# Kernel tuning notes

Hardware: AMD Instinct MI355X
Metric: run time of the kernel (lower is better)

Reference implementation:

```python
import jax, jax.numpy as jnp
import numpy as np

N, T, D, H = 64, 512, 1024, 1024

def setup_inputs() -> dict:
    key = jax.random.key(0)
    k1, k2, k3, k4 = jax.random.split(key, 4)
    x = jax.random.normal(k1, (N, T, D), dtype=jnp.float32)
    h0 = jax.random.normal(k2, (N, H), dtype=jnp.float32)
    Wx = jax.random.normal(k3, (D, H), dtype=jnp.float32) / np.sqrt(D)
    Wh = jax.random.normal(k4, (H, H), dtype=jnp.float32) / np.sqrt(H)
    b = jnp.zeros((H,), dtype=jnp.float32)
    return {"x": x, "h0": h0, "Wx": Wx, "Wh": Wh, "b": b}

def reference(x, h0, Wx, Wh, b):
    # Precompute input projection for all timesteps in one big GEMM: (N,T,D)@(D,H) -> (N,T,H)
    xW = jnp.einsum('ntd,dh->nth', x, Wx) + b
    xW_t = jnp.swapaxes(xW, 0, 1)  # (T, N, H)

    def step(prev_h, xw):
        next_h = jnp.tanh(prev_h @ Wh + xw)
        return next_h, next_h

    _, h_t = jax.lax.scan(step, h0, xW_t)  # h_t: (T, N, H)
    return jnp.swapaxes(h_t, 0, 1)  # (N, T, H)
```

## Files before the change

kernel.cpp:

```cpp
#include <hip/hip_runtime.h>

#define NB 64
#define TT 512
#define DD 1024
#define HH 1024

typedef unsigned long long u64;
typedef __attribute__((ext_vector_type(4))) float f32x4;
typedef __attribute__((ext_vector_type(8))) short bf16x8;

static __device__ __forceinline__ unsigned short f2bf(float f) {
  unsigned u = __float_as_uint(f);
  unsigned r = (u + 0x7fffu + ((u >> 16) & 1u)) >> 16;
  return (unsigned short)r;
}
static __device__ __forceinline__ float bf2f(unsigned short u) {
  return __uint_as_float(((unsigned)u) << 16);
}
static __device__ __forceinline__ float ftanh(float x) {
  float z = __builtin_amdgcn_exp2f(x * 2.8853900817779268f);
  return 1.f - 2.f * __builtin_amdgcn_rcpf(z + 1.f);
}
static __device__ __forceinline__ void async_copy16(void* lds, const void* g) {
  __builtin_amdgcn_global_load_lds(
      (const __attribute__((address_space(1))) unsigned int*)g,
      (__attribute__((address_space(3))) unsigned int*)lds, 16, 0, 0);
}

__global__ __launch_bounds__(256) void prep_kernel(
    const float* __restrict__ x, const float* __restrict__ Wx,
    const float* __restrict__ h0, unsigned short* __restrict__ Wxh,
    unsigned short* __restrict__ Wxl, unsigned short* __restrict__ hbuf0,
    unsigned short* __restrict__ xbf, int nx, int permuted) {
  __shared__ float tile[32][33];
  int b = blockIdx.x;
  int tid = threadIdx.x;
  if (b < nx) {
    int g = b * 256 + tid;
    int r = g >> 7, jb = g & 127;
    int q = jb >> 3, j = jb & 7;
    const float4* src = (const float4*)(x + r * 1024 + jb * 8);
    float4 a0 = src[0], a1 = src[1];
    uint4 o;
    o.x = (unsigned)f2bf(a0.x) | ((unsigned)f2bf(a0.y) << 16);
    o.y = (unsigned)f2bf(a0.z) | ((unsigned)f2bf(a0.w) << 16);
    o.z = (unsigned)f2bf(a1.x) | ((unsigned)f2bf(a1.y) << 16);
    o.w = (unsigned)f2bf(a1.z) | ((unsigned)f2bf(a1.w) << 16);
    *(uint4*)((char*)xbf + (size_t)r * 2048 + q * 128 + ((j ^ (r & 7)) << 4)) = o;
  } else if (b < nx + 1024) {
    int bb = b - nx;
    int tk = (bb & 31) * 32;
    int tn = (bb >> 5) * 32;
    int tx = tid & 31;
    int ty = tid >> 5;
#pragma unroll
    for (int ii = 0; ii < 4; ++ii) {
      int kk = ty + ii * 8;
      tile[kk][tx] = Wx[(tk + kk) * HH + tn + tx];
    }
    __syncthreads();
#pragma unroll
    for (int ii = 0; ii < 4; ++ii) {
      int a = ty + ii * 8;
      float wv = tile[tx][a];
      unsigned short hi = f2bf(wv);
      float lo = wv - bf2f(hi);
      int c = tn + a, k = tk + tx;
      int idx;
      if (permuted) {
        int qq = k >> 6, e = k & 63, j = e >> 3;
        idx = c * 1024 + qq * 64 + ((j ^ (c & 7)) << 3) + (e & 7);
      } else {
        idx = c * 1024 + k;
      }
      Wxh[idx] = hi;
      Wxl[idx] = f2bf(lo);
    }
  } else {
    int i = (b - nx - 1024) * 256 + tid;
    int n = i >> 7, cb = i & 127;
    const float4* s4 = (const float4*)(h0 + n * 1024 + cb * 8);
    float4 a0 = s4[0], a1 = s4[1];
    uint4 o;
    o.x = (unsigned)f2bf(a0.x) | ((unsigned)f2bf(a0.y) << 16);
    o.y = (unsigned)f2bf(a0.z) | ((unsigned)f2bf(a0.w) << 16);
    o.z = (unsigned)f2bf(a1.x) | ((unsigned)f2bf(a1.y) << 16);
    o.w = (unsigned)f2bf(a1.z) | ((unsigned)f2bf(a1.w) << 16);
    *(uint4*)((char*)hbuf0 + (size_t)n * 2048 + cb * 16) = o;
  }
}

__global__ __launch_bounds__(256) void xw_gemm_fast(
    const unsigned short* __restrict__ xbf,
    const unsigned short* __restrict__ Wxh,
    const unsigned short* __restrict__ Wxl, const float* __restrict__ bias,
    float* __restrict__ out) {
  __shared__ unsigned short As[128 * 64];
  __shared__ unsigned short Bh[128 * 64];
  __shared__ unsigned short Bl[128 * 64];
  int tid = threadIdx.x;
  int w = tid >> 6, lane = tid & 63;
  int n0 = blockIdx.x * 128, row0 = blockIdx.y * 128;
  int wr = w >> 1, wc = w & 1;

  f32x4 acc[4][4];
#pragma unroll
  for (int m = 0; m < 4; ++m)
#pragma unroll
    for (int n = 0; n < 4; ++n) acc[m][n] = (f32x4)0.f;

  const char* xb = (const char*)xbf;
  const char* hb = (const char*)Wxh;
  const char* lb = (const char*)Wxl;

  for (int kc = 0; kc < 16; ++kc) {
    __syncthreads();
#pragma unroll
    for (int i = 0; i < 4; ++i) {
      int ub = i * 4096 + w * 1024;
      int off = ub + lane * 16;
      int r = off >> 7, inrow = off & 127;
      async_copy16((char*)As + ub,
                   xb + (size_t)(row0 + r) * 2048 + kc * 128 + inrow);
    }
#pragma unroll
    for (int i = 0; i < 4; ++i) {
      int ub = i * 4096 + w * 1024;
      int off = ub + lane * 16;
      int c = off >> 7, inrow = off & 127;
      async_copy16((char*)Bh + ub,
                   hb + (size_t)(n0 + c) * 2048 + kc * 128 + inrow);
      async_copy16((char*)Bl + ub,
                   lb + (size_t)(n0 + c) * 2048 + kc * 128 + inrow);
    }
    asm volatile("s_waitcnt vmcnt(0)" ::: "memory");
    __syncthreads();
#pragma unroll
    for (int kt = 0; kt < 2; ++kt) {
      int krel2 = (kt * 32 + ((lane >> 4) << 3)) * 2;
      bf16x8 af[4], bhf[4], blf[4];
#pragma unroll
      for (int m = 0; m < 4; ++m) {
        int r = wr * 64 + m * 16 + (lane & 15);
        af[m] = *(const bf16x8*)((const char*)As + r * 128 +
                                 (krel2 ^ ((r & 7) << 4)));
      }
#pragma unroll
      for (int n = 0; n < 4; ++n) {
        int c = wc * 64 + n * 16 + (lane & 15);
        int off = c * 128 + (krel2 ^ ((c & 7) << 4));
        bhf[n] = *(const bf16x8*)((const char*)Bh + off);
        blf[n] = *(const bf16x8*)((const char*)Bl + off);
      }
#pragma unroll
      for (int m = 0; m < 4; ++m)
#pragma unroll
        for (int n = 0; n < 4; ++n) {
          acc[m][n] = __builtin_amdgcn_mfma_f32_16x16x32_bf16(af[m], bhf[n],
                                                              acc[m][n], 0, 0, 0);
          acc[m][n] = __builtin_amdgcn_mfma_f32_16x16x32_bf16(af[m], blf[n],
                                                              acc[m][n], 0, 0, 0);
        }
    }
  }

#pragma unroll
  for (int n = 0; n < 4; ++n) {
    int col = n0 + wc * 64 + n * 16 + (lane & 15);
    float bv = bias[col];
#pragma unroll
    for (int m = 0; m < 4; ++m) {
      int rbase = row0 + wr * 64 + m * 16 + ((lane >> 4) << 2);
#pragma unroll
      for (int i = 0; i < 4; ++i)
        out[(size_t)(rbase + i) * HH + col] = acc[m][n][i] + bv;
    }
  }
}

__global__ __launch_bounds__(256) void xw_gemm_slow(
    const float* __restrict__ x, const unsigned short* __restrict__ Wxh,
    const unsigned short* __restrict__ Wxl, const float* __restrict__ bias,
    float* __restrict__ out) {
  __shared__ unsigned short As[128 * 64];
  __shared__ unsigned short Bh[128 * 64];
  __shared__ unsigned short Bl[128 * 64];

  int tid = threadIdx.x;
  int n0 = blockIdx.x * 128;
  int row0 = blockIdx.y * 128;
  int w = tid >> 6, lane = tid & 63;
  int wr = w >> 1, wc = w & 1;

  f32x4 acc[4][4];
#pragma unroll
  for (int m = 0; m < 4; ++m)
#pragma unroll
    for (int n = 0; n < 4; ++n) acc[m][n] = (f32x4)0.f;

  for (int kk = 0; kk < DD; kk += 64) {
    float4 av[8];
#pragma unroll
    for (int i = 0; i < 8; ++i) {
      int lin = tid + 256 * i;
      int r = lin >> 4, kq = lin & 15;
      av[i] = *(const float4*)(x + (size_t)(row0 + r) * DD + kk + kq * 4);
    }
    int4 bhv[4], blv[4];
#pragma unroll
    for (int i = 0; i < 4; ++i) {
      int lin = tid + 256 * i;
      int c = lin >> 3, kb = lin & 7;
      bhv[i] = *(const int4*)(Wxh + (size_t)(n0 + c) * DD + kk + kb * 8);
      blv[i] = *(const int4*)(Wxl + (size_t)(n0 + c) * DD + kk + kb * 8);
    }
    __syncthreads();
#pragma unroll
    for (int i = 0; i < 8; ++i) {
      int lin = tid + 256 * i;
      int r = lin >> 4, kq = lin & 15;
      uint2 u;
      u.x = (unsigned)f2bf(av[i].x) | ((unsigned)f2bf(av[i].y) << 16);
      u.y = (unsigned)f2bf(av[i].z) | ((unsigned)f2bf(av[i].w) << 16);
      *(uint2*)((char*)As + r * 128 + ((kq * 8) ^ ((r & 7) << 4))) = u;
    }
#pragma unroll
    for (int i = 0; i < 4; ++i) {
      int lin = tid + 256 * i;
      int c = lin >> 3, kb = lin & 7;
      int off = c * 128 + ((kb * 16) ^ ((c & 7) << 4));
      *(int4*)((char*)Bh + off) = bhv[i];
      *(int4*)((char*)Bl + off) = blv[i];
    }
    __syncthreads();
#pragma unroll
    for (int kt = 0; kt < 2; ++kt) {
      int krel2 = (kt * 32 + ((lane >> 4) << 3)) * 2;
      bf16x8 af[4], bhf[4], blf[4];
#pragma unroll
      for (int m = 0; m < 4; ++m) {
        int r = wr * 64 + m * 16 + (lane & 15);
        af[m] = *(const bf16x8*)((const char*)As + r * 128 +
                                 (krel2 ^ ((r & 7) << 4)));
      }
#pragma unroll
      for (int n = 0; n < 4; ++n) {
        int c = wc * 64 + n * 16 + (lane & 15);
        int off = c * 128 + (krel2 ^ ((c & 7) << 4));
        bhf[n] = *(const bf16x8*)((const char*)Bh + off);
        blf[n] = *(const bf16x8*)((const char*)Bl + off);
      }
#pragma unroll
      for (int m = 0; m < 4; ++m)
#pragma unroll
        for (int n = 0; n < 4; ++n) {
          acc[m][n] = __builtin_amdgcn_mfma_f32_16x16x32_bf16(af[m], bhf[n],
                                                              acc[m][n], 0, 0, 0);
          acc[m][n] = __builtin_amdgcn_mfma_f32_16x16x32_bf16(af[m], blf[n],
                                                              acc[m][n], 0, 0, 0);
        }
    }
    __syncthreads();
  }

#pragma unroll
  for (int n = 0; n < 4; ++n) {
    int col = n0 + wc * 64 + n * 16 + (lane & 15);
    float bv = bias[col];
#pragma unroll
    for (int m = 0; m < 4; ++m) {
      int rbase = row0 + wr * 64 + m * 16 + ((lane >> 4) << 2);
#pragma unroll
      for (int i = 0; i < 4; ++i)
        out[(size_t)(rbase + i) * HH + col] = acc[m][n][i] + bv;
    }
  }
}

__global__ __launch_bounds__(256) void rnn_scan(
    const float* __restrict__ Wh, float* __restrict__ out,
    unsigned short* __restrict__ hbuf, unsigned* __restrict__ flags) {
  int tid = threadIdx.x;
  int w = tid >> 6, lane = tid & 63;
  int p = blockIdx.x >> 4;
  int q = blockIdx.x & 15;
  int n0 = p * 16;
  int c0 = q * 64;

  __shared__ float red[2][4][16][68];

  bf16x8 whi[4][8], wlo[4][8];
#pragma unroll
  for (int ct = 0; ct < 4; ++ct) {
#pragma unroll
    for (int kt = 0; kt < 8; ++kt) {
      int c = c0 + ct * 16 + (lane & 15);
      int kb = w * 256 + kt * 32 + ((lane >> 4) << 3);
#pragma unroll
      for (int j = 0; j < 8; ++j) {
        float wf = Wh[(size_t)(kb + j) * HH + c];
        unsigned short hi = f2bf(wf);
        whi[ct][kt][j] = (short)hi;
        wlo[ct][kt][j] = (short)f2bf(wf - bf2f(hi));
      }
    }
  }

  int erow_l = tid >> 4;
  int erow = n0 + erow_l;
  int ecol = c0 + ((tid & 15) << 2);
  size_t obase = (size_t)erow * (TT * HH) + ecol;
  int hbase = erow * HH + ecol;
  int abase = (n0 + (lane & 15)) * HH + w * 256 + ((lane >> 4) << 3);

  unsigned* myflag = flags + p * 64 + q * 4 + w;
  const unsigned* pollp = flags + p * 64 + lane;

  float4 xw0 = *(const float4*)(out + obase);
  float4 xw1 = *(const float4*)(out + obase + HH);
  float4 prev_hv = make_float4(0.f, 0.f, 0.f, 0.f);

  for (int t = 0; t < TT; ++t) {
    const unsigned short* hp = hbuf + (t & 1) * (NB * HH);
    unsigned short* hn = hbuf + ((t + 1) & 1) * (NB * HH);

    if (t > 0) {
      unsigned tg = (unsigned)t;
      for (;;) {
        unsigned v = __hip_atomic_load(pollp, __ATOMIC_RELAXED,
                                       __HIP_MEMORY_SCOPE_AGENT);
        if (__all((int)(v >= tg))) break;
        __builtin_amdgcn_s_sleep(1);
      }
      asm volatile("" ::: "memory");
    }

    const u64* hq = (const u64*)(hp + abase);
    u64 pu[8][2];
#pragma unroll
    for (int kt = 0; kt < 8; ++kt) {
      pu[kt][0] = __hip_atomic_load(hq + kt * 8, __ATOMIC_RELAXED,
                                    __HIP_MEMORY_SCOPE_AGENT);
      pu[kt][1] = __hip_atomic_load(hq + kt * 8 + 1, __ATOMIC_RELAXED,
                                    __HIP_MEMORY_SCOPE_AGENT);
    }

    f32x4 acc[4];
#pragma unroll
    for (int ct = 0; ct < 4; ++ct) acc[ct] = (f32x4)0.f;
#pragma unroll
    for (int kt = 0; kt < 8; ++kt) {
      union { u64 u[2]; bf16x8 v; } pk;
      pk.u[0] = pu[kt][0];
      pk.u[1] = pu[kt][1];
#pragma unroll
      for (int ct = 0; ct < 4; ++ct) {
        acc[ct] = __builtin_amdgcn_mfma_f32_16x16x32_bf16(pk.v, whi[ct][kt],
                                                          acc[ct], 0, 0, 0);
        acc[ct] = __builtin_amdgcn_mfma_f32_16x16x32_bf16(pk.v, wlo[ct][kt],
                                                          acc[ct], 0, 0, 0);
      }
    }

    int db = t & 1;
    int rr = (lane >> 4) << 2, cc = lane & 15;
#pragma unroll
    for (int ct = 0; ct < 4; ++ct)
#pragma unroll
      for (int i = 0; i < 4; ++i) red[db][w][rr + i][ct * 16 + cc] = acc[ct][i];
    asm volatile("s_waitcnt lgkmcnt(0)" ::: "memory");
    __builtin_amdgcn_s_barrier();
    asm volatile("" ::: "memory");

    int c4 = (tid & 15) << 2;
    float4 s = make_float4(0.f, 0.f, 0.f, 0.f);
#pragma unroll
    for (int ww = 0; ww < 4; ++ww) {
      float4 v = *(const float4*)&red[db][ww][erow_l][c4];
      s.x += v.x; s.y += v.y; s.z += v.z; s.w += v.w;
    }
    float4 hv;
    hv.x = ftanh(s.x + xw0.x);
    hv.y = ftanh(s.y + xw0.y);
    hv.z = ftanh(s.z + xw0.z);
    hv.w = ftanh(s.w + xw0.w);

    if (t + 1 < TT) {
      unsigned lo32 = (unsigned)f2bf(hv.x) | ((unsigned)f2bf(hv.y) << 16);
      unsigned hi32 = (unsigned)f2bf(hv.z) | ((unsigned)f2bf(hv.w) << 16);
      __hip_atomic_store((u64*)(hn + hbase), ((u64)hi32 << 32) | lo32,
                         __ATOMIC_RELAXED, __HIP_MEMORY_SCOPE_AGENT);
      asm volatile("s_waitcnt vmcnt(0)" ::: "memory");
      if (lane == 0)
        __hip_atomic_store(myflag, (unsigned)(t + 1), __ATOMIC_RELAXED,
                           __HIP_MEMORY_SCOPE_AGENT);
    }

    if (t > 0) *(float4*)(out + obase + (size_t)(t - 1) * HH) = prev_hv;
    prev_hv = hv;
    float4 xwf = make_float4(0.f, 0.f, 0.f, 0.f);
    if (t + 2 < TT) xwf = *(const float4*)(out + obase + (size_t)(t + 2) * HH);
    xw0 = xw1;
    xw1 = xwf;
  }
  *(float4*)(out + obase + (size_t)(TT - 1) * HH) = prev_hv;
}

extern "C" void kernel_launch(void* const* d_in, const int* in_sizes, int n_in,
                              void* d_out, int out_size, void* d_ws,
                              size_t ws_size, hipStream_t stream) {
  const float* x = (const float*)d_in[0];
  const float* h0 = (const float*)d_in[1];
  const float* Wx = (const float*)d_in[2];
  const float* Wh = (const float*)d_in[3];
  const float* b = (const float*)d_in[4];
  float* out = (float*)d_out;

  char* ws = (char*)d_ws;
  unsigned* flags = (unsigned*)ws;
  unsigned short* hbuf = (unsigned short*)(ws + 4096);
  unsigned short* Wxh = (unsigned short*)(ws + 266240);
  unsigned short* Wxl = (unsigned short*)(ws + 2363392);
  unsigned short* xbf = (unsigned short*)(ws + 4460544);

  int fast = (ws_size >= 71569408ULL) ? 1 : 0;
  int nx = fast ? 16384 : 0;

  hipMemsetAsync(flags, 0, 4096, stream);
  prep_kernel<<<nx + 1056, 256, 0, stream>>>(x, Wx, h0, Wxh, Wxl, hbuf, xbf,
                                             nx, fast);
  if (fast)
    xw_gemm_fast<<<dim3(8, 256), 256, 0, stream>>>(xbf, Wxh, Wxl, b, out);
  else
    xw_gemm_slow<<<dim3(8, 256), 256, 0, stream>>>(x, Wxh, Wxl, b, out);
  rnn_scan<<<64, 256, 0, stream>>>(Wh, out, hbuf, flags);
}
```

Measured before the change: 2.297 ms.

## Replace flag polling with timestamp-tagged hidden-state words in a 4-deep ring buffer

The separate per-wave flag array and its poll/store handshake are removed. Each 64-bit hidden-state word now carries two bf16 values in its low half and the timestep tag in its high half. Consumers spin on the data loads themselves until every tag matches, and the buffer becomes a 4-slot ring so a slot is not overwritten while slower blocks still read it. This drops a round trip and the vmcnt wait before each flag store on the serial critical path, at the cost of twice the hidden-state traffic and repeated re-reads of the full operand while spinning. The output store and the xw prefetch are also moved ahead of the MFMA work.

```diff
diff --git a/kernel.cpp b/kernel.cpp
--- a/kernel.cpp
+++ b/kernel.cpp
@@ -30,7 +30,7 @@
 __global__ __launch_bounds__(256) void prep_kernel(
     const float* __restrict__ x, const float* __restrict__ Wx,
     const float* __restrict__ h0, unsigned short* __restrict__ Wxh,
-    unsigned short* __restrict__ Wxl, unsigned short* __restrict__ hbuf0,
+    unsigned short* __restrict__ Wxl, u64* __restrict__ hbuf,
     unsigned short* __restrict__ xbf, int nx, int permuted) {
   __shared__ float tile[32][33];
   int b = blockIdx.x;
@@ -77,16 +77,13 @@
       Wxl[idx] = f2bf(lo);
     }
   } else {
-    int i = (b - nx - 1024) * 256 + tid;
-    int n = i >> 7, cb = i & 127;
-    const float4* s4 = (const float4*)(h0 + n * 1024 + cb * 8);
-    float4 a0 = s4[0], a1 = s4[1];
-    uint4 o;
-    o.x = (unsigned)f2bf(a0.x) | ((unsigned)f2bf(a0.y) << 16);
-    o.y = (unsigned)f2bf(a0.z) | ((unsigned)f2bf(a0.w) << 16);
-    o.z = (unsigned)f2bf(a1.x) | ((unsigned)f2bf(a1.y) << 16);
-    o.w = (unsigned)f2bf(a1.z) | ((unsigned)f2bf(a1.w) << 16);
-    *(uint4*)((char*)hbuf0 + (size_t)n * 2048 + cb * 16) = o;
+    int pi = (b - nx - 1024) * 256 + tid;
+    int n = pi >> 9, c2 = pi & 511;
+    float v0 = h0[n * HH + c2 * 2];
+    float v1 = h0[n * HH + c2 * 2 + 1];
+    unsigned lo32 = (unsigned)f2bf(v0) | ((unsigned)f2bf(v1) << 16);
+    __hip_atomic_store(hbuf + pi, (u64)lo32, __ATOMIC_RELAXED,
+                       __HIP_MEMORY_SCOPE_AGENT);
   }
 }
 
@@ -279,7 +276,7 @@
 
 __global__ __launch_bounds__(256) void rnn_scan(
     const float* __restrict__ Wh, float* __restrict__ out,
-    unsigned short* __restrict__ hbuf, unsigned* __restrict__ flags) {
+    u64* __restrict__ hbuf) {
   int tid = threadIdx.x;
   int w = tid >> 6, lane = tid & 63;
   int p = blockIdx.x >> 4;
@@ -310,54 +307,47 @@
   int erow = n0 + erow_l;
   int ecol = c0 + ((tid & 15) << 2);
   size_t obase = (size_t)erow * (TT * HH) + ecol;
-  int hbase = erow * HH + ecol;
-  int abase = (n0 + (lane & 15)) * HH + w * 256 + ((lane >> 4) << 3);
-
-  unsigned* myflag = flags + p * 64 + q * 4 + w;
-  const unsigned* pollp = flags + p * 64 + lane;
+  int pstore = (p * 16 + erow_l) * 512 + (ecol >> 1);
+  int pload = (p * 16 + (lane & 15)) * 512 + w * 128 + ((lane >> 4) << 2);
 
   float4 xw0 = *(const float4*)(out + obase);
   float4 xw1 = *(const float4*)(out + obase + HH);
   float4 prev_hv = make_float4(0.f, 0.f, 0.f, 0.f);
 
   for (int t = 0; t < TT; ++t) {
-    const unsigned short* hp = hbuf + (t & 1) * (NB * HH);
-    unsigned short* hn = hbuf + ((t + 1) & 1) * (NB * HH);
-
-    if (t > 0) {
-      unsigned tg = (unsigned)t;
-      for (;;) {
-        unsigned v = __hip_atomic_load(pollp, __ATOMIC_RELAXED,
-                                       __HIP_MEMORY_SCOPE_AGENT);
-        if (__all((int)(v >= tg))) break;
-        __builtin_amdgcn_s_sleep(1);
-      }
-      asm volatile("" ::: "memory");
-    }
-
-    const u64* hq = (const u64*)(hp + abase);
-    u64 pu[8][2];
+    const u64* hq = hbuf + (unsigned)(t & 3) * 32768 + pload;
+    u64* hn = hbuf + (unsigned)((t + 1) & 3) * 32768;
+    unsigned tg = (unsigned)t;
+
+    u64 pk[32];
+    for (;;) {
+#pragma unroll
+      for (int i = 0; i < 32; ++i)
+        pk[i] = __hip_atomic_load(hq + (i >> 2) * 16 + (i & 3),
+                                  __ATOMIC_RELAXED, __HIP_MEMORY_SCOPE_AGENT);
+      unsigned bad = 0;
+#pragma unroll
+      for (int i = 0; i < 32; ++i) bad |= (unsigned)(pk[i] >> 32) ^ tg;
+      if (__all((int)(bad == 0))) break;
+    }
+
+    if (t > 0) *(float4*)(out + obase + (size_t)(t - 1) * HH) = prev_hv;
+    float4 xwf = make_float4(0.f, 0.f, 0.f, 0.f);
+    if (t + 2 < TT) xwf = *(const float4*)(out + obase + (size_t)(t + 2) * HH);
+
+    f32x4 acc[4];
+#pragma unroll
+    for (int ct = 0; ct < 4; ++ct) acc[ct] = (f32x4)0.f;
 #pragma unroll
     for (int kt = 0; kt < 8; ++kt) {
-      pu[kt][0] = __hip_atomic_load(hq + kt * 8, __ATOMIC_RELAXED,
-                                    __HIP_MEMORY_SCOPE_AGENT);
-      pu[kt][1] = __hip_atomic_load(hq + kt * 8 + 1, __ATOMIC_RELAXED,
-                                    __HIP_MEMORY_SCOPE_AGENT);
-    }
-
-    f32x4 acc[4];
-#pragma unroll
-    for (int ct = 0; ct < 4; ++ct) acc[ct] = (f32x4)0.f;
-#pragma unroll
-    for (int kt = 0; kt < 8; ++kt) {
-      union { u64 u[2]; bf16x8 v; } pk;
-      pk.u[0] = pu[kt][0];
-      pk.u[1] = pu[kt][1];
+      union { unsigned u[4]; bf16x8 v; } pkk;
+#pragma unroll
+      for (int j = 0; j < 4; ++j) pkk.u[j] = (unsigned)pk[kt * 4 + j];
 #pragma unroll
       for (int ct = 0; ct < 4; ++ct) {
-        acc[ct] = __builtin_amdgcn_mfma_f32_16x16x32_bf16(pk.v, whi[ct][kt],
+        acc[ct] = __builtin_amdgcn_mfma_f32_16x16x32_bf16(pkk.v, whi[ct][kt],
                                                           acc[ct], 0, 0, 0);
-        acc[ct] = __builtin_amdgcn_mfma_f32_16x16x32_bf16(pk.v, wlo[ct][kt],
+        acc[ct] = __builtin_amdgcn_mfma_f32_16x16x32_bf16(pkk.v, wlo[ct][kt],
                                                           acc[ct], 0, 0, 0);
       }
     }
@@ -386,20 +376,15 @@
     hv.w = ftanh(s.w + xw0.w);
 
     if (t + 1 < TT) {
-      unsigned lo32 = (unsigned)f2bf(hv.x) | ((unsigned)f2bf(hv.y) << 16);
-      unsigned hi32 = (unsigned)f2bf(hv.z) | ((unsigned)f2bf(hv.w) << 16);
-      __hip_atomic_store((u64*)(hn + hbase), ((u64)hi32 << 32) | lo32,
-                         __ATOMIC_RELAXED, __HIP_MEMORY_SCOPE_AGENT);
-      asm volatile("s_waitcnt vmcnt(0)" ::: "memory");
-      if (lane == 0)
-        __hip_atomic_store(myflag, (unsigned)(t + 1), __ATOMIC_RELAXED,
-                           __HIP_MEMORY_SCOPE_AGENT);
-    }
-
-    if (t > 0) *(float4*)(out + obase + (size_t)(t - 1) * HH) = prev_hv;
+      u64 thi = ((u64)(unsigned)(t + 1)) << 32;
+      unsigned lo0 = (unsigned)f2bf(hv.x) | ((unsigned)f2bf(hv.y) << 16);
+      unsigned lo1 = (unsigned)f2bf(hv.z) | ((unsigned)f2bf(hv.w) << 16);
+      __hip_atomic_store(hn + pstore, thi | lo0, __ATOMIC_RELAXED,
+                         __HIP_MEMORY_SCOPE_AGENT);
+      __hip_atomic_store(hn + pstore + 1, thi | lo1, __ATOMIC_RELAXED,
+                         __HIP_MEMORY_SCOPE_AGENT);
+    }
     prev_hv = hv;
-    float4 xwf = make_float4(0.f, 0.f, 0.f, 0.f);
-    if (t + 2 < TT) xwf = *(const float4*)(out + obase + (size_t)(t + 2) * HH);
     xw0 = xw1;
     xw1 = xwf;
   }
@@ -417,21 +402,20 @@
   float* out = (float*)d_out;
 
   char* ws = (char*)d_ws;
-  unsigned* flags = (unsigned*)ws;
-  unsigned short* hbuf = (unsigned short*)(ws + 4096);
-  unsigned short* Wxh = (unsigned short*)(ws + 266240);
-  unsigned short* Wxl = (unsigned short*)(ws + 2363392);
-  unsigned short* xbf = (unsigned short*)(ws + 4460544);
-
-  int fast = (ws_size >= 71569408ULL) ? 1 : 0;
+  u64* hbuf = (u64*)(ws + 4096);
+  unsigned short* Wxh = (unsigned short*)(ws + 1052672);
+  unsigned short* Wxl = (unsigned short*)(ws + 3149824);
+  unsigned short* xbf = (unsigned short*)(ws + 5246976);
+
+  int fast = (ws_size >= 72355840ULL) ? 1 : 0;
   int nx = fast ? 16384 : 0;
 
-  hipMemsetAsync(flags, 0, 4096, stream);
-  prep_kernel<<<nx + 1056, 256, 0, stream>>>(x, Wx, h0, Wxh, Wxl, hbuf, xbf,
+  hipMemsetAsync(hbuf, 0, 1048576, stream);
+  prep_kernel<<<nx + 1152, 256, 0, stream>>>(x, Wx, h0, Wxh, Wxl, hbuf, xbf,
                                              nx, fast);
   if (fast)
     xw_gemm_fast<<<dim3(8, 256), 256, 0, stream>>>(xbf, Wxh, Wxl, b, out);
   else
     xw_gemm_slow<<<dim3(8, 256), 256, 0, stream>>>(x, Wxh, Wxl, b, out);
-  rnn_scan<<<64, 256, 0, stream>>>(Wh, out, hbuf, flags);
-}
+  rnn_scan<<<64, 256, 0, stream>>>(Wh, out, hbuf);
+}
```

Measured after the change: 3.198 ms. 39.2% more time.

## Aggregate per-block step flags via LDS counter and poll only dependent blocks

Applied to the files above, without the earlier changes.

Each block now publishes a single step flag. The last of its four waves to finish, found through an LDS atomic counter, writes it, instead of every wave writing its own flag. Each wave polls only the four producer blocks whose columns feed its K-slice, rather than all 64 wave flags of the batch group. This narrows the cross-block dependency and cuts polling traffic. The code also drops the two-step xW prefetch and the delayed output store, so the xW load and output store now happen inside each step. The output store is also now covered by the vmcnt(0) wait before the flag is published, which may lengthen the critical path.

```diff
diff --git a/kernel.cpp b/kernel.cpp
--- a/kernel.cpp
+++ b/kernel.cpp
@@ -288,6 +288,8 @@
   int c0 = q * 64;
 
   __shared__ float red[2][4][16][68];
+  __shared__ unsigned cnt;
+  if (tid == 0) cnt = 0u;
 
   bf16x8 whi[4][8], wlo[4][8];
 #pragma unroll
@@ -305,6 +307,7 @@
       }
     }
   }
+  __syncthreads();
 
   int erow_l = tid >> 4;
   int erow = n0 + erow_l;
@@ -313,12 +316,8 @@
   int hbase = erow * HH + ecol;
   int abase = (n0 + (lane & 15)) * HH + w * 256 + ((lane >> 4) << 3);
 
-  unsigned* myflag = flags + p * 64 + q * 4 + w;
-  const unsigned* pollp = flags + p * 64 + lane;
-
-  float4 xw0 = *(const float4*)(out + obase);
-  float4 xw1 = *(const float4*)(out + obase + HH);
-  float4 prev_hv = make_float4(0.f, 0.f, 0.f, 0.f);
+  unsigned* myflag = flags + p * 64 + q;
+  const unsigned* fp = flags + p * 64 + (w << 2);
 
   for (int t = 0; t < TT; ++t) {
     const unsigned short* hp = hbuf + (t & 1) * (NB * HH);
@@ -327,13 +326,17 @@
     if (t > 0) {
       unsigned tg = (unsigned)t;
       for (;;) {
-        unsigned v = __hip_atomic_load(pollp, __ATOMIC_RELAXED,
-                                       __HIP_MEMORY_SCOPE_AGENT);
-        if (__all((int)(v >= tg))) break;
+        unsigned fv = 0xFFFFFFFFu;
+        if (lane < 4)
+          fv = __hip_atomic_load(fp + lane, __ATOMIC_RELAXED,
+                                 __HIP_MEMORY_SCOPE_AGENT);
+        if (__all((int)(fv >= tg))) break;
         __builtin_amdgcn_s_sleep(1);
       }
       asm volatile("" ::: "memory");
     }
+
+    float4 xwc = *(const float4*)(out + obase + (size_t)t * HH);
 
     const u64* hq = (const u64*)(hp + abase);
     u64 pu[8][2];
@@ -380,10 +383,12 @@
       s.x += v.x; s.y += v.y; s.z += v.z; s.w += v.w;
     }
     float4 hv;
-    hv.x = ftanh(s.x + xw0.x);
-    hv.y = ftanh(s.y + xw0.y);
-    hv.z = ftanh(s.z + xw0.z);
-    hv.w = ftanh(s.w + xw0.w);
+    hv.x = ftanh(s.x + xwc.x);
+    hv.y = ftanh(s.y + xwc.y);
+    hv.z = ftanh(s.z + xwc.z);
+    hv.w = ftanh(s.w + xwc.w);
+
+    *(float4*)(out + obase + (size_t)t * HH) = hv;
 
     if (t + 1 < TT) {
       unsigned lo32 = (unsigned)f2bf(hv.x) | ((unsigned)f2bf(hv.y) << 16);
@@ -391,19 +396,14 @@
       __hip_atomic_store((u64*)(hn + hbase), ((u64)hi32 << 32) | lo32,
                          __ATOMIC_RELAXED, __HIP_MEMORY_SCOPE_AGENT);
       asm volatile("s_waitcnt vmcnt(0)" ::: "memory");
-      if (lane == 0)
-        __hip_atomic_store(myflag, (unsigned)(t + 1), __ATOMIC_RELAXED,
-                           __HIP_MEMORY_SCOPE_AGENT);
-    }
-
-    if (t > 0) *(float4*)(out + obase + (size_t)(t - 1) * HH) = prev_hv;
-    prev_hv = hv;
-    float4 xwf = make_float4(0.f, 0.f, 0.f, 0.f);
-    if (t + 2 < TT) xwf = *(const float4*)(out + obase + (size_t)(t + 2) * HH);
-    xw0 = xw1;
-    xw1 = xwf;
-  }
-  *(float4*)(out + obase + (size_t)(TT - 1) * HH) = prev_hv;
+      if (lane == 0) {
+        unsigned old = atomicAdd(&cnt, 1u);
+        if (old == 4u * (unsigned)t + 3u)
+          __hip_atomic_store(myflag, (unsigned)(t + 1), __ATOMIC_RELAXED,
+                             __HIP_MEMORY_SCOPE_AGENT);
+      }
+    }
+  }
 }
 
 extern "C" void kernel_launch(void* const* d_in, const int* in_sizes, int n_in,
```

Measured after the change: 2.660 ms. 1.16x slower.
